# Kernel tuning notes

Hardware: AMD Instinct MI355X
Metric: run time of the kernel (lower is better)

The kernel has to match this reference:

```python
import jax, jax.numpy as jnp
import numpy as np

EPS = 1e-6
BASE_CURVATURE = 1.0


def _artanh(x):
    return jnp.arctanh(jnp.clip(x, -1.0 + 1e-5, 1.0 - 1e-5))


def _norm(x):
    return jnp.maximum(jnp.linalg.norm(x, axis=-1, keepdims=True), EPS)


def _logmap0(x, c):
    # Poincare-ball log map at origin
    sc = jnp.sqrt(c)
    n = _norm(x)
    return _artanh(sc * n) * x / (sc * n)


def _expmap0(v, c):
    # Poincare-ball exp map at origin
    sc = jnp.sqrt(c)
    n = _norm(v)
    return jnp.tanh(sc * n) * v / (sc * n)


def _mobius_add(x, y, c):
    x2 = jnp.sum(x * x, axis=-1, keepdims=True)
    y2 = jnp.sum(y * y, axis=-1, keepdims=True)
    xy = jnp.sum(x * y, axis=-1, keepdims=True)
    num = (1.0 + 2.0 * c * xy + c * y2) * x + (1.0 - c * x2) * y
    den = 1.0 + 2.0 * c * xy + (c * c) * x2 * y2
    return num / jnp.maximum(den, EPS)


def _mobius_scalar_mul(t, x, c):
    sc = jnp.sqrt(c)
    n = _norm(x)
    return jnp.tanh(t * _artanh(sc * n)) * x / (sc * n)


def setup_inputs() -> dict:
    key = jax.random.key(0)
    ks = jax.random.split(key, 8)
    B, D_in, D_out, K = 4096, 2048, 2048, 4
    scale_w = np.sqrt(2.0 / (D_in + D_out)) * 0.1
    return {
        "x": jax.random.normal(ks[0], (B, D_in), jnp.float32) * 0.05,
        "weight": jax.random.normal(ks[1], (D_out, D_in), jnp.float32) * scale_w,
        "bias": jax.random.normal(ks[2], (D_out,), jnp.float32) * 0.01,
        "curv_weight": jax.random.normal(ks[3], (1, D_in), jnp.float32) * 0.1,
        "curv_bias": jnp.zeros((1,), jnp.float32),
        "anchors": jax.random.normal(ks[4], (K, D_out), jnp.float32) * 0.3,
        "t_values": jnp.full((K,), 0.5, jnp.float32),
        "anchor_weights": jnp.full((K,), 1.0 / K, jnp.float32),
    }


def reference(x, weight, bias, curv_weight, curv_bias, anchors, t_values, anchor_weights):
    # 1) dynamic curvature prediction: c_i = base_c * softplus(x . w + b), then mean
    logits = x @ curv_weight[0] + curv_bias[0]                 # [B]
    curvatures = BASE_CURVATURE * jax.nn.softplus(logits)      # [B]
    c = jax.lax.stop_gradient(jnp.mean(curvatures))            # scalar (.item() in torch)

    # 2) fused hyperbolic linear: expmap0(logmap0(x) @ W^T + b)
    u = _logmap0(x, c)                                         # [B, D_in]
    h = u @ weight.T + bias                                    # [B, D_out]
    y = _expmap0(h, c)                                         # [B, D_out]

    # 3) geodesic activation: weighted Mobius geodesic toward each anchor
    xe = y[:, None, :]                                         # [B, 1, D]
    a = anchors[None, :, :]                                    # [1, K, D]
    diff = _mobius_add(-xe, a, c)                              # [B, K, D]
    step = _mobius_scalar_mul(t_values[None, :, None], diff, c)
    g = _mobius_add(xe, step, c)                               # [B, K, D]
    w = jax.nn.softmax(anchor_weights)                         # [K]
    return jnp.einsum("bkd,k->bd", g, w)                       # [B, D_out]
```

## Files before the change

### kernel.cpp

```cpp
#include <hip/hip_runtime.h>
#include <stdint.h>

#define B_ROWS 4096
#define D_IN   2048
#define D_OUT  2048
#define KANCH  4
#define MROWS  8

typedef _Float16 half8  __attribute__((ext_vector_type(8)));
typedef _Float16 half4  __attribute__((ext_vector_type(4)));
typedef float    floatx4 __attribute__((ext_vector_type(4)));
typedef const __attribute__((address_space(1))) uint8_t* gptr_t;
typedef __attribute__((address_space(3))) uint8_t* lptr_t;

__device__ __forceinline__ float frcp(float x)   { return __builtin_amdgcn_rcpf(x); }
__device__ __forceinline__ float ftanh(float x)  { float e = __expf(2.f * x); return (e - 1.f) * frcp(e + 1.f); }
__device__ __forceinline__ float fatanh(float z) { return 0.5f * __logf((1.f + z) * frcp(1.f - z)); }

__global__ __launch_bounds__(256) void k_prep(
    const float* __restrict__ x,
    const float* __restrict__ W,
    const float* __restrict__ cw,
    const float* __restrict__ cb,
    const float* __restrict__ bias,
    const float* __restrict__ anchors,
    _Float16* __restrict__ xh,
    _Float16* __restrict__ Wh,
    float* __restrict__ n2x,
    float* __restrict__ spart,
    float* __restrict__ scal)
{
    int tid = threadIdx.x;
    if (blockIdx.x < 1024) {
        int w = tid >> 6, lane = tid & 63;
        int row = blockIdx.x * 4 + w;
        const floatx4* xr = (const floatx4*)(x + (size_t)row * D_IN);
        const floatx4* wr = (const floatx4*)cw;
        _Float16* xo = xh + (size_t)row * D_IN;
        float dot = 0.f, ss = 0.f;
#pragma unroll
        for (int i = 0; i < 8; ++i) {
            int idx = i * 64 + lane;
            floatx4 xv = xr[idx];
            floatx4 wv = wr[idx];
#pragma unroll
            for (int j = 0; j < 4; ++j) {
                dot += xv[j] * wv[j];
                ss  += xv[j] * xv[j];
            }
            half4 h = {(_Float16)xv[0], (_Float16)xv[1], (_Float16)xv[2], (_Float16)xv[3]};
            *(half4*)(xo + idx * 4) = h;
        }
#pragma unroll
        for (int off = 32; off; off >>= 1) {
            dot += __shfl_down(dot, off);
            ss  += __shfl_down(ss, off);
        }
        __shared__ float spw[4];
        if (lane == 0) {
            n2x[row] = ss;
            float z = dot + cb[0];
            spw[w] = (z > 20.f) ? z : log1pf(expf(z));
        }
        __syncthreads();
        if (tid == 0)
            spart[blockIdx.x] = spw[0] + spw[1] + spw[2] + spw[3];
    } else if (blockIdx.x < 2048) {
        int blk = blockIdx.x - 1024;
        const floatx4* W4 = (const floatx4*)W;
#pragma unroll
        for (int i = 0; i < 4; ++i) {
            int idx = blk * 1024 + i * 256 + tid;
            floatx4 v = W4[idx];
            half4 h = {(_Float16)v[0], (_Float16)v[1], (_Float16)v[2], (_Float16)v[3]};
            *(half4*)(Wh + (size_t)idx * 4) = h;
        }
    } else {
        int w = tid >> 6, lane = tid & 63;
        float bf[8], af[KANCH][8];
        *(floatx4*)(bf)     = *(const floatx4*)(bias + tid * 8);
        *(floatx4*)(bf + 4) = *(const floatx4*)(bias + tid * 8 + 4);
#pragma unroll
        for (int k = 0; k < KANCH; ++k) {
            *(floatx4*)(af[k])     = *(const floatx4*)(anchors + (size_t)k * D_OUT + tid * 8);
            *(floatx4*)(af[k] + 4) = *(const floatx4*)(anchors + (size_t)k * D_OUT + tid * 8 + 4);
        }
        float v[9];
#pragma unroll
        for (int q = 0; q < 9; ++q) v[q] = 0.f;
#pragma unroll
        for (int j = 0; j < 8; ++j) {
            v[0] += bf[j] * bf[j];
#pragma unroll
            for (int k = 0; k < KANCH; ++k) {
                v[1 + k] += bf[j] * af[k][j];
                v[5 + k] += af[k][j] * af[k][j];
            }
        }
#pragma unroll
        for (int off = 32; off; off >>= 1)
#pragma unroll
            for (int q = 0; q < 9; ++q) v[q] += __shfl_down(v[q], off);
        __shared__ float red[4][9];
        if (lane == 0)
#pragma unroll
            for (int q = 0; q < 9; ++q) red[w][q] = v[q];
        __syncthreads();
        if (tid == 0)
#pragma unroll
            for (int q = 0; q < 9; ++q)
                scal[1 + q] = red[0][q] + red[1][q] + red[2][q] + red[3][q];
    }
}

template<int KPB>
__global__ __launch_bounds__(512, 2) void k_gemm(
    const _Float16* __restrict__ A,
    const _Float16* __restrict__ W,
    _Float16* __restrict__ P0,
    _Float16* __restrict__ P1)
{
    constexpr int NT = KPB / 64;
    constexpr int NZ = (KPB == D_IN) ? 1 : 2;
    __shared__ __align__(16) _Float16 lds[2][2][2][8192];
    const int tid  = threadIdx.x;
    const int lane = tid & 63;
    const int w    = tid >> 6;
    const int wm   = w >> 2;
    const int wn   = w & 3;

    int lin = (blockIdx.z * gridDim.y + blockIdx.y) * gridDim.x + blockIdx.x;
    int xcd = lin & 7;
    int i   = lin >> 3;
    int zz, mt, nt;
    if (NZ == 2) {
        zz = xcd & 1;
        int grp = xcd >> 1;
        mt = (grp >> 1) * 8 + (i >> 2);
        nt = (grp & 1) * 4 + (i & 3);
    } else {
        zz = 0;
        mt = (xcd >> 1) * 4 + (i >> 2);
        nt = (xcd & 1) * 4 + (i & 3);
    }
    const int bm0 = mt * 256;
    const int bn0 = nt * 256;
    const int kbase = zz * KPB;
    _Float16* P = (zz == 0) ? P0 : P1;

    const int e0 = tid * 16;
    const int srow = w * 16 + (lane & 15);
    const int scol = (lane >> 4) * 8;
    const size_t asrc = (size_t)(bm0 + srow) * D_IN + scol + kbase;
    const size_t bsrc = (size_t)(bn0 + srow) * D_IN + scol + kbase;
    const int wmoff = wm * 8192;
    const int wnoff = wn * 4096;
    const int loff  = lane * 16;

#define STAGE_Q(OP, D, KH, GP, SRC, KB) do { \
    uint8_t* qb_ = (uint8_t*)&lds[OP][D][KH][0]; \
    __builtin_amdgcn_global_load_lds((gptr_t)((GP) + (SRC) + (KB)), (lptr_t)(qb_ + e0), 16, 0, 0); \
    __builtin_amdgcn_global_load_lds((gptr_t)((GP) + (SRC) + (size_t)128 * D_IN + (KB)), (lptr_t)(qb_ + e0 + 8192), 16, 0, 0); \
} while (0)

    floatx4 acc[8][4];
#pragma unroll
    for (int mi = 0; mi < 8; ++mi)
#pragma unroll
        for (int ni = 0; ni < 4; ++ni)
            acc[mi][ni] = (floatx4){0.f, 0.f, 0.f, 0.f};

    STAGE_Q(0, 0, 0, A, asrc, 0);
    STAGE_Q(0, 0, 1, A, asrc, 32);
    STAGE_Q(1, 0, 0, W, bsrc, 0);
    STAGE_Q(1, 0, 1, W, bsrc, 32);
    STAGE_Q(0, 1, 0, A, asrc, 64);
    STAGE_Q(1, 1, 0, W, bsrc, 64);
    STAGE_Q(1, 1, 1, W, bsrc, 96);
    asm volatile("s_waitcnt vmcnt(6)" ::: "memory");
    __builtin_amdgcn_s_barrier();

    half8 aq[4], bq[4];

#define LOAD_A4(D, KH, MI0) do { _Pragma("unroll") \
    for (int mi = 0; mi < 4; ++mi) \
        aq[mi] = *(const half8*)((const uint8_t*)&lds[0][D][KH][0] + wmoff + ((MI0) + mi) * 1024 + loff); \
} while (0)
#define LOAD_B4(D, KH) do { _Pragma("unroll") \
    for (int ni = 0; ni < 4; ++ni) \
        bq[ni] = *(const half8*)((const uint8_t*)&lds[1][D][KH][0] + wnoff + ni * 1024 + loff); \
} while (0)
#define MFMA16(MI0) do { \
    __builtin_amdgcn_s_barrier(); \
    __builtin_amdgcn_s_setprio(1); \
    _Pragma("unroll") for (int mi = 0; mi < 4; ++mi) \
    _Pragma("unroll") for (int ni = 0; ni < 4; ++ni) \
        acc[(MI0) + mi][ni] = __builtin_amdgcn_mfma_f32_16x16x32_f16(aq[mi], bq[ni], acc[(MI0) + mi][ni], 0, 0, 0); \
    __builtin_amdgcn_s_setprio(0); \
} while (0)
#define ENDPH() __builtin_amdgcn_s_barrier()

#define TILE_BODY(T, D) do { \
    LOAD_A4(D, 0, 0); LOAD_B4(D, 0); \
    if ((T) + 1 < NT) STAGE_Q(0, (D) ^ 1, 1, A, asrc, ((T) + 1) * 64 + 32); \
    MFMA16(0); ENDPH(); \
    LOAD_A4(D, 0, 4); \
    if ((T) + 2 < NT) STAGE_Q(1, D, 0, W, bsrc, ((T) + 2) * 64); \
    MFMA16(4); ENDPH(); \
    LOAD_A4(D, 1, 0); LOAD_B4(D, 1); \
    if ((T) + 2 < NT) STAGE_Q(0, D, 0, A, asrc, ((T) + 2) * 64); \
    MFMA16(0); ENDPH(); \
    LOAD_A4(D, 1, 4); \
    if ((T) + 2 < NT) STAGE_Q(1, D, 1, W, bsrc, ((T) + 2) * 64 + 32); \
    MFMA16(4); \
    if ((T) < NT - 2) asm volatile("s_waitcnt vmcnt(6)" ::: "memory"); \
    else              asm volatile("s_waitcnt vmcnt(0)" ::: "memory"); \
    ENDPH(); \
} while (0)

    for (int t = 0; t < NT; t += 2) {
        TILE_BODY(t, 0);
        TILE_BODY(t + 1, 1);
    }

#undef TILE_BODY
#undef ENDPH
#undef MFMA16
#undef LOAD_B4
#undef LOAD_A4
#undef STAGE_Q

#pragma unroll
    for (int mi = 0; mi < 8; ++mi) {
#pragma unroll
        for (int r = 0; r < 4; ++r) {
            int gm = bm0 + wm * 128 + mi * 16 + (lane >> 4) * 4 + r;
#pragma unroll
            for (int ni = 0; ni < 4; ++ni) {
                int gn = bn0 + wn * 64 + ni * 16 + (lane & 15);
                P[(size_t)gm * D_OUT + gn] = (_Float16)acc[mi][ni][r];
            }
        }
    }
}

__global__ __launch_bounds__(256) void k_mobius(
    const _Float16* __restrict__ P0,
    const _Float16* __restrict__ P1,
    const float* __restrict__ bias,
    const float* __restrict__ anchors,
    const float* __restrict__ tv,
    const float* __restrict__ aw,
    const float* __restrict__ n2x,
    const float* __restrict__ spart,
    const float* __restrict__ scal,
    int split,
    float* __restrict__ out)
{
    int tid = threadIdx.x, w = tid >> 6, lane = tid & 63;
    float bf[8];
    *(floatx4*)(bf)     = *(const floatx4*)(bias + tid * 8);
    *(floatx4*)(bf + 4) = *(const floatx4*)(bias + tid * 8 + 4);
    float af[KANCH][8];
#pragma unroll
    for (int k = 0; k < KANCH; ++k) {
        *(floatx4*)(af[k])     = *(const floatx4*)(anchors + (size_t)k * D_OUT + tid * 8);
        *(floatx4*)(af[k] + 4) = *(const floatx4*)(anchors + (size_t)k * D_OUT + tid * 8 + 4);
    }
    float v6;
    {
        floatx4 s4 = ((const floatx4*)spart)[tid];
        v6 = s4[0] + s4[1] + s4[2] + s4[3];
    }
#pragma unroll
    for (int off = 32; off; off >>= 1) v6 += __shfl_down(v6, off);
    __shared__ float redS[4];
    __shared__ float red[4][6];
    __shared__ float cf[2 + KANCH];
    if (lane == 0) redS[w] = v6;
    __syncthreads();

    int k = lane & 3;
    float c = 0.f, sc = 0.f, wk = 0.f, tvk = 0.f, bb = 0.f, ba = 0.f, aa = 0.f;
    if (w == 0) {
        float spsum = redS[0] + redS[1] + redS[2] + redS[3];
        c  = spsum * (1.0f / (float)B_ROWS);
        sc = __builtin_amdgcn_sqrtf(c);
        float ek = __expf(aw[k]);
        float se = ek;
        se += __shfl_xor(se, 1);
        se += __shfl_xor(se, 2);
        wk = ek * frcp(se);
        tvk = tv[k];
        bb = scal[1];
        ba = scal[2 + k];
        aa = scal[6 + k];
    }

    for (int r = 0; r < MROWS; ++r) {
        int row = blockIdx.x * MROWS + r;
        size_t rowoff = (size_t)row * D_OUT;
        float pf[8];
        {
            half8 p = *(const half8*)(P0 + rowoff + tid * 8);
#pragma unroll
            for (int j = 0; j < 8; ++j) pf[j] = (float)p[j];
        }
        if (split == 2) {
            half8 q = *(const half8*)(P1 + rowoff + tid * 8);
#pragma unroll
            for (int j = 0; j < 8; ++j) pf[j] += (float)q[j];
        }
        float v[6];
#pragma unroll
        for (int q = 0; q < 6; ++q) v[q] = 0.f;
#pragma unroll
        for (int j = 0; j < 8; ++j) {
            v[0] += pf[j] * pf[j];
            v[1] += pf[j] * bf[j];
#pragma unroll
            for (int kk = 0; kk < KANCH; ++kk) v[2 + kk] += pf[j] * af[kk][j];
        }
#pragma unroll
        for (int off = 32; off; off >>= 1)
#pragma unroll
            for (int q = 0; q < 6; ++q) v[q] += __shfl_down(v[q], off);
        if (lane == 0)
#pragma unroll
            for (int q = 0; q < 6; ++q) red[w][q] = v[q];
        __syncthreads();
        if (w == 0) {
            float pp = red[0][0] + red[1][0] + red[2][0] + red[3][0];
            float pb = red[0][1] + red[1][1] + red[2][1] + red[3][1];
            float pa = red[0][2 + k] + red[1][2 + k] + red[2][2 + k] + red[3][2 + k];
            float nx = fmaxf(__builtin_amdgcn_sqrtf(n2x[row]), 1e-6f);
            float ax = sc * nx;
            float zx = fminf(fmaxf(ax, -1.f + 1e-5f), 1.f - 1e-5f);
            float f = fatanh(zx) * frcp(ax);
            float hh = f * f * pp + 2.f * f * pb + bb;
            float ha = f * pa + ba;
            float nh = fmaxf(__builtin_amdgcn_sqrtf(hh), 1e-6f);
            float snh = sc * nh;
            float gy = ftanh(snh) * frcp(snh);
            float x2 = gy * gy * hh;
            float B1 = 1.f - c * x2;
            float y2 = aa;
            float dy = gy * ha;
            float A1 = 1.f - 2.f * c * dy + c * y2;
            float den1 = fmaxf(1.f - 2.f * c * dy + c * c * x2 * y2, 1e-6f);
            float rd1 = frcp(den1);
            float al = -A1 * rd1, be = B1 * rd1;
            float nd2 = fmaxf(al * al * x2 + 2.f * al * be * dy + be * be * y2, 0.f);
            float nd = fmaxf(__builtin_amdgcn_sqrtf(nd2), 1e-6f);
            float snd = sc * nd;
            float zc = fminf(fmaxf(snd, -1.f + 1e-5f), 1.f - 1e-5f);
            float s = ftanh(tvk * fatanh(zc)) * frcp(snd);
            float y2s = s * s * nd2;
            float xys = s * (al * x2 + be * dy);
            float A2 = 1.f + 2.f * c * xys + c * y2s;
            float den2 = fmaxf(1.f + 2.f * c * xys + c * c * x2 * y2s, 1e-6f);
            float rd2 = frcp(den2);
            float Cy  = (A2 + B1 * s * al) * rd2;
            float Cak = (B1 * s * be) * rd2;
            float chk = wk * Cy;
            chk += __shfl_xor(chk, 1);
            chk += __shfl_xor(chk, 2);
            if (lane == 0) {
                float c0 = gy * chk;
                cf[0] = c0 * f;
                cf[1] = c0;
            }
            if (lane < 4) cf[2 + lane] = wk * Cak;
        }
        __syncthreads();
        float cp = cf[0], cb_ = cf[1];
        float o[8];
#pragma unroll
        for (int j = 0; j < 8; ++j) {
            float val = cp * pf[j] + cb_ * bf[j];
#pragma unroll
            for (int kk = 0; kk < KANCH; ++kk) val += cf[2 + kk] * af[kk][j];
            o[j] = val;
        }
        *(floatx4*)(out + rowoff + tid * 8)     = *(floatx4*)(o);
        *(floatx4*)(out + rowoff + tid * 8 + 4) = *(floatx4*)(o + 4);
    }
}

extern "C" void kernel_launch(void* const* d_in, const int* in_sizes, int n_in,
                              void* d_out, int out_size, void* d_ws, size_t ws_size,
                              hipStream_t stream) {
    const float* x       = (const float*)d_in[0];
    const float* wt      = (const float*)d_in[1];
    const float* bias    = (const float*)d_in[2];
    const float* cw      = (const float*)d_in[3];
    const float* cb      = (const float*)d_in[4];
    const float* anchors = (const float*)d_in[5];
    const float* tv      = (const float*)d_in[6];
    const float* aw      = (const float*)d_in[7];
    float* out = (float*)d_out;

    _Float16* Wh = (_Float16*)d_ws;
    _Float16* xh = Wh + (size_t)D_OUT * D_IN;
    float* n2x   = (float*)(xh + (size_t)B_ROWS * D_IN);
    float* spart = n2x + B_ROWS;
    float* scal  = spart + 1024;
    _Float16* P0 = (_Float16*)(scal + 16);
    _Float16* P1 = P0 + (size_t)B_ROWS * D_OUT;
    size_t need2 = (size_t)((char*)(P1 + (size_t)B_ROWS * D_OUT) - (char*)d_ws);
    int split = (ws_size >= need2) ? 2 : 1;

    k_prep<<<2049, 256, 0, stream>>>(x, wt, cw, cb, bias, anchors, xh, Wh, n2x, spart, scal);
    if (split == 2)
        k_gemm<D_IN / 2><<<dim3(8, 16, 2), 512, 0, stream>>>(xh, Wh, P0, P1);
    else
        k_gemm<D_IN><<<dim3(8, 16, 1), 512, 0, stream>>>(xh, Wh, P0, P1);
    k_mobius<<<B_ROWS / MROWS, 256, 0, stream>>>(P0, P1, bias, anchors, tv, aw, n2x, spart, scal, split, out);
}
```

Before: 168.6 us.

## Fuse prep, GEMM and Mobius epilogue into one cooperative kernel with grid syncs

Replaces the three separate launches (prep, split-K GEMM, Mobius epilogue) with a single cooperative kernel of 256 blocks, using grid.sync between phases. Prep work is redistributed so each block converts 16 x-rows and 8 W-rows, and the epilogue processes 16 rows per block with 512 threads. This removes two kernel launch gaps and inter-kernel drain/fill overhead, at the cost of grid-wide barriers and a coarser, less parallel prep and epilogue phase (256 blocks instead of 2049/512). The fallback path keeps separate kernels and adds an extra syncthreads in the Mobius loop.

Result: slower. 266.7 us (+58.2%).

```diff
diff --git a/kernel.cpp b/kernel.cpp
--- a/kernel.cpp
+++ b/kernel.cpp
@@ -1,4 +1,5 @@
 #include <hip/hip_runtime.h>
+#include <hip/hip_cooperative_groups.h>
 #include <stdint.h>
 
 #define B_ROWS 4096
@@ -7,6 +8,8 @@
 #define KANCH  4
 #define MROWS  8
 
+namespace cg = cooperative_groups;
+
 typedef _Float16 half8  __attribute__((ext_vector_type(8)));
 typedef _Float16 half4  __attribute__((ext_vector_type(4)));
 typedef float    floatx4 __attribute__((ext_vector_type(4)));
@@ -17,18 +20,367 @@
 __device__ __forceinline__ float ftanh(float x)  { float e = __expf(2.f * x); return (e - 1.f) * frcp(e + 1.f); }
 __device__ __forceinline__ float fatanh(float z) { return 0.5f * __logf((1.f + z) * frcp(1.f - z)); }
 
-__global__ __launch_bounds__(256) void k_prep(
+__global__ __launch_bounds__(512, 2) void k_mega(
     const float* __restrict__ x,
     const float* __restrict__ W,
+    const float* __restrict__ bias,
     const float* __restrict__ cw,
     const float* __restrict__ cb,
-    const float* __restrict__ bias,
     const float* __restrict__ anchors,
+    const float* __restrict__ tv,
+    const float* __restrict__ aw,
     _Float16* __restrict__ xh,
     _Float16* __restrict__ Wh,
     float* __restrict__ n2x,
     float* __restrict__ spart,
-    float* __restrict__ scal)
+    float* __restrict__ scal,
+    _Float16* __restrict__ P0,
+    _Float16* __restrict__ P1,
+    float* __restrict__ out)
+{
+    __shared__ __align__(16) _Float16 lds[2][2][2][8192];
+    float* scr = (float*)&lds[0][0][0][0];
+
+    const int tid  = threadIdx.x;
+    const int lane = tid & 63;
+    const int w    = tid >> 6;
+    const int lin  = (blockIdx.z * gridDim.y + blockIdx.y) * gridDim.x + blockIdx.x;
+
+    cg::grid_group grid = cg::this_grid();
+
+    {
+        const floatx4* wr4 = (const floatx4*)cw;
+        floatx4 wv[8];
+#pragma unroll
+        for (int i = 0; i < 8; ++i) wv[i] = wr4[i * 64 + lane];
+        float sp = 0.f;
+#pragma unroll
+        for (int rr = 0; rr < 2; ++rr) {
+            int row = lin * 16 + w * 2 + rr;
+            const floatx4* xr = (const floatx4*)(x + (size_t)row * D_IN);
+            _Float16* xo = xh + (size_t)row * D_IN;
+            float dot = 0.f, ss = 0.f;
+#pragma unroll
+            for (int i = 0; i < 8; ++i) {
+                int idx = i * 64 + lane;
+                floatx4 xv = xr[idx];
+#pragma unroll
+                for (int j = 0; j < 4; ++j) {
+                    dot += xv[j] * wv[i][j];
+                    ss  += xv[j] * xv[j];
+                }
+                half4 h = {(_Float16)xv[0], (_Float16)xv[1], (_Float16)xv[2], (_Float16)xv[3]};
+                *(half4*)(xo + idx * 4) = h;
+            }
+#pragma unroll
+            for (int off = 32; off; off >>= 1) {
+                dot += __shfl_down(dot, off);
+                ss  += __shfl_down(ss, off);
+            }
+            if (lane == 0) {
+                n2x[row] = ss;
+                float z = dot + cb[0];
+                sp += (z > 20.f) ? z : log1pf(expf(z));
+            }
+        }
+        if (lane == 0) scr[w] = sp;
+
+        {
+            int wrow = lin * 8 + w;
+            const floatx4* W4 = (const floatx4*)(W + (size_t)wrow * D_IN);
+            _Float16* wo = Wh + (size_t)wrow * D_IN;
+#pragma unroll
+            for (int i = 0; i < 8; ++i) {
+                int idx = i * 64 + lane;
+                floatx4 v = W4[idx];
+                half4 h = {(_Float16)v[0], (_Float16)v[1], (_Float16)v[2], (_Float16)v[3]};
+                *(half4*)(wo + idx * 4) = h;
+            }
+        }
+
+        float v9[9];
+#pragma unroll
+        for (int q = 0; q < 9; ++q) v9[q] = 0.f;
+        if (lin == 0) {
+            floatx4 bv = *(const floatx4*)(bias + tid * 4);
+            floatx4 av[KANCH];
+#pragma unroll
+            for (int k = 0; k < KANCH; ++k)
+                av[k] = *(const floatx4*)(anchors + (size_t)k * D_OUT + tid * 4);
+#pragma unroll
+            for (int j = 0; j < 4; ++j) {
+                v9[0] += bv[j] * bv[j];
+#pragma unroll
+                for (int k = 0; k < KANCH; ++k) {
+                    v9[1 + k] += bv[j] * av[k][j];
+                    v9[5 + k] += av[k][j] * av[k][j];
+                }
+            }
+#pragma unroll
+            for (int off = 32; off; off >>= 1)
+#pragma unroll
+                for (int q = 0; q < 9; ++q) v9[q] += __shfl_down(v9[q], off);
+            if (lane == 0)
+#pragma unroll
+                for (int q = 0; q < 9; ++q) scr[8 + w * 9 + q] = v9[q];
+        }
+        __syncthreads();
+        if (tid == 0) {
+            spart[lin] = scr[0] + scr[1] + scr[2] + scr[3] + scr[4] + scr[5] + scr[6] + scr[7];
+            if (lin == 0) {
+#pragma unroll
+                for (int q = 0; q < 9; ++q) {
+                    float s = 0.f;
+#pragma unroll
+                    for (int ww = 0; ww < 8; ++ww) s += scr[8 + ww * 9 + q];
+                    scal[1 + q] = s;
+                }
+            }
+        }
+    }
+
+    grid.sync();
+
+    {
+        constexpr int KPB = D_IN / 2;
+        constexpr int NT  = KPB / 64;
+        const int wm = w >> 2;
+        const int wn = w & 3;
+
+        int xcd = lin & 7;
+        int i   = lin >> 3;
+        int zz  = xcd & 1;
+        int grp = xcd >> 1;
+        int mt  = (grp >> 1) * 8 + (i >> 2);
+        int nt  = (grp & 1) * 4 + (i & 3);
+        const int bm0 = mt * 256;
+        const int bn0 = nt * 256;
+        const int kbase = zz * KPB;
+        _Float16* P = (zz == 0) ? P0 : P1;
+
+        const int e0 = tid * 16;
+        const int srow = w * 16 + (lane & 15);
+        const int scol = (lane >> 4) * 8;
+        const size_t asrc = (size_t)(bm0 + srow) * D_IN + scol + kbase;
+        const size_t bsrc = (size_t)(bn0 + srow) * D_IN + scol + kbase;
+        const int wmoff = wm * 8192;
+        const int wnoff = wn * 4096;
+        const int loff  = lane * 16;
+
+#define STAGE_Q(OP, D, KH, GP, SRC, KB) do { \
+    uint8_t* qb_ = (uint8_t*)&lds[OP][D][KH][0]; \
+    __builtin_amdgcn_global_load_lds((gptr_t)((GP) + (SRC) + (KB)), (lptr_t)(qb_ + e0), 16, 0, 0); \
+    __builtin_amdgcn_global_load_lds((gptr_t)((GP) + (SRC) + (size_t)128 * D_IN + (KB)), (lptr_t)(qb_ + e0 + 8192), 16, 0, 0); \
+} while (0)
+
+        floatx4 acc[8][4];
+#pragma unroll
+        for (int mi = 0; mi < 8; ++mi)
+#pragma unroll
+            for (int ni = 0; ni < 4; ++ni)
+                acc[mi][ni] = (floatx4){0.f, 0.f, 0.f, 0.f};
+
+        STAGE_Q(0, 0, 0, xh, asrc, 0);
+        STAGE_Q(0, 0, 1, xh, asrc, 32);
+        STAGE_Q(1, 0, 0, Wh, bsrc, 0);
+        STAGE_Q(1, 0, 1, Wh, bsrc, 32);
+        STAGE_Q(0, 1, 0, xh, asrc, 64);
+        STAGE_Q(1, 1, 0, Wh, bsrc, 64);
+        STAGE_Q(1, 1, 1, Wh, bsrc, 96);
+        asm volatile("s_waitcnt vmcnt(6)" ::: "memory");
+        __builtin_amdgcn_s_barrier();
+
+        half8 aq[4], bq[4];
+
+#define LOAD_A4(D, KH, MI0) do { _Pragma("unroll") \
+    for (int mi = 0; mi < 4; ++mi) \
+        aq[mi] = *(const half8*)((const uint8_t*)&lds[0][D][KH][0] + wmoff + ((MI0) + mi) * 1024 + loff); \
+} while (0)
+#define LOAD_B4(D, KH) do { _Pragma("unroll") \
+    for (int ni = 0; ni < 4; ++ni) \
+        bq[ni] = *(const half8*)((const uint8_t*)&lds[1][D][KH][0] + wnoff + ni * 1024 + loff); \
+} while (0)
+#define MFMA16(MI0) do { \
+    __builtin_amdgcn_s_barrier(); \
+    __builtin_amdgcn_s_setprio(1); \
+    _Pragma("unroll") for (int mi = 0; mi < 4; ++mi) \
+    _Pragma("unroll") for (int ni = 0; ni < 4; ++ni) \
+        acc[(MI0) + mi][ni] = __builtin_amdgcn_mfma_f32_16x16x32_f16(aq[mi], bq[ni], acc[(MI0) + mi][ni], 0, 0, 0); \
+    __builtin_amdgcn_s_setprio(0); \
+} while (0)
+#define ENDPH() __builtin_amdgcn_s_barrier()
+
+#define TILE_BODY(T, D) do { \
+    LOAD_A4(D, 0, 0); LOAD_B4(D, 0); \
+    if ((T) + 1 < NT) STAGE_Q(0, (D) ^ 1, 1, xh, asrc, ((T) + 1) * 64 + 32); \
+    MFMA16(0); ENDPH(); \
+    LOAD_A4(D, 0, 4); \
+    if ((T) + 2 < NT) STAGE_Q(1, D, 0, Wh, bsrc, ((T) + 2) * 64); \
+    MFMA16(4); ENDPH(); \
+    LOAD_A4(D, 1, 0); LOAD_B4(D, 1); \
+    if ((T) + 2 < NT) STAGE_Q(0, D, 0, xh, asrc, ((T) + 2) * 64); \
+    MFMA16(0); ENDPH(); \
+    LOAD_A4(D, 1, 4); \
+    if ((T) + 2 < NT) STAGE_Q(1, D, 1, Wh, bsrc, ((T) + 2) * 64 + 32); \
+    MFMA16(4); \
+    if ((T) < NT - 2) asm volatile("s_waitcnt vmcnt(6)" ::: "memory"); \
+    else              asm volatile("s_waitcnt vmcnt(0)" ::: "memory"); \
+    ENDPH(); \
+} while (0)
+
+        for (int t = 0; t < NT; t += 2) {
+            TILE_BODY(t, 0);
+            TILE_BODY(t + 1, 1);
+        }
+
+#undef TILE_BODY
+#undef ENDPH
+#undef MFMA16
+#undef LOAD_B4
+#undef LOAD_A4
+#undef STAGE_Q
+
+#pragma unroll
+        for (int mi = 0; mi < 8; ++mi) {
+#pragma unroll
+            for (int r = 0; r < 4; ++r) {
+                int gm = bm0 + wm * 128 + mi * 16 + (lane >> 4) * 4 + r;
+#pragma unroll
+                for (int ni = 0; ni < 4; ++ni) {
+                    int gn = bn0 + wn * 64 + ni * 16 + (lane & 15);
+                    P[(size_t)gm * D_OUT + gn] = (_Float16)acc[mi][ni][r];
+                }
+            }
+        }
+    }
+
+    grid.sync();
+
+    {
+        float bf4[4];
+        *(floatx4*)bf4 = *(const floatx4*)(bias + tid * 4);
+        float af4[KANCH][4];
+#pragma unroll
+        for (int k = 0; k < KANCH; ++k)
+            *(floatx4*)af4[k] = *(const floatx4*)(anchors + (size_t)k * D_OUT + tid * 4);
+
+        int k = lane & 3;
+        float c = 0.f, sc = 0.f, wk = 0.f, tvk = 0.f, bb = 0.f, ba = 0.f, aa = 0.f;
+        if (w == 0) {
+            floatx4 s4 = ((const floatx4*)spart)[lane];
+            float v6 = s4[0] + s4[1] + s4[2] + s4[3];
+#pragma unroll
+            for (int off = 32; off; off >>= 1) v6 += __shfl_down(v6, off);
+            float spsum = __shfl(v6, 0);
+            c  = spsum * (1.0f / (float)B_ROWS);
+            sc = __builtin_amdgcn_sqrtf(c);
+            float ek = __expf(aw[k]);
+            float se = ek;
+            se += __shfl_xor(se, 1);
+            se += __shfl_xor(se, 2);
+            wk = ek * frcp(se);
+            tvk = tv[k];
+            bb = scal[1];
+            ba = scal[2 + k];
+            aa = scal[6 + k];
+        }
+
+        for (int r = 0; r < 16; ++r) {
+            int row = lin * 16 + r;
+            size_t rowoff = (size_t)row * D_OUT;
+            float pf[4];
+            {
+                half4 p0 = *(const half4*)(P0 + rowoff + tid * 4);
+                half4 p1 = *(const half4*)(P1 + rowoff + tid * 4);
+#pragma unroll
+                for (int j = 0; j < 4; ++j) pf[j] = (float)p0[j] + (float)p1[j];
+            }
+            float v[6];
+#pragma unroll
+            for (int q = 0; q < 6; ++q) v[q] = 0.f;
+#pragma unroll
+            for (int j = 0; j < 4; ++j) {
+                v[0] += pf[j] * pf[j];
+                v[1] += pf[j] * bf4[j];
+#pragma unroll
+                for (int kk = 0; kk < KANCH; ++kk) v[2 + kk] += pf[j] * af4[kk][j];
+            }
+#pragma unroll
+            for (int off = 32; off; off >>= 1)
+#pragma unroll
+                for (int q = 0; q < 6; ++q) v[q] += __shfl_down(v[q], off);
+            if (lane == 0)
+#pragma unroll
+                for (int q = 0; q < 6; ++q) scr[8 + w * 6 + q] = v[q];
+            __syncthreads();
+            if (w == 0) {
+                float pp = 0.f, pb = 0.f, pa = 0.f;
+#pragma unroll
+                for (int ww = 0; ww < 8; ++ww) {
+                    pp += scr[8 + ww * 6 + 0];
+                    pb += scr[8 + ww * 6 + 1];
+                    pa += scr[8 + ww * 6 + 2 + k];
+                }
+                float nx = fmaxf(__builtin_amdgcn_sqrtf(n2x[row]), 1e-6f);
+                float ax = sc * nx;
+                float zx = fminf(fmaxf(ax, -1.f + 1e-5f), 1.f - 1e-5f);
+                float f = fatanh(zx) * frcp(ax);
+                float hh = f * f * pp + 2.f * f * pb + bb;
+                float ha = f * pa + ba;
+                float nh = fmaxf(__builtin_amdgcn_sqrtf(hh), 1e-6f);
+                float snh = sc * nh;
+                float gy = ftanh(snh) * frcp(snh);
+                float x2 = gy * gy * hh;
+                float B1 = 1.f - c * x2;
+                float y2 = aa;
+                float dy = gy * ha;
+                float A1 = 1.f - 2.f * c * dy + c * y2;
+                float den1 = fmaxf(1.f - 2.f * c * dy + c * c * x2 * y2, 1e-6f);
+                float rd1 = frcp(den1);
+                float al = -A1 * rd1, be = B1 * rd1;
+                float nd2 = fmaxf(al * al * x2 + 2.f * al * be * dy + be * be * y2, 0.f);
+                float nd = fmaxf(__builtin_amdgcn_sqrtf(nd2), 1e-6f);
+                float snd = sc * nd;
+                float zc = fminf(fmaxf(snd, -1.f + 1e-5f), 1.f - 1e-5f);
+                float s = ftanh(tvk * fatanh(zc)) * frcp(snd);
+                float y2s = s * s * nd2;
+                float xys = s * (al * x2 + be * dy);
+                float A2 = 1.f + 2.f * c * xys + c * y2s;
+                float den2 = fmaxf(1.f + 2.f * c * xys + c * c * x2 * y2s, 1e-6f);
+                float rd2 = frcp(den2);
+                float Cy  = (A2 + B1 * s * al) * rd2;
+                float Cak = (B1 * s * be) * rd2;
+                float chk = wk * Cy;
+                chk += __shfl_xor(chk, 1);
+                chk += __shfl_xor(chk, 2);
+                if (lane == 0) {
+                    float c0 = gy * chk;
+                    scr[0] = c0 * f;
+                    scr[1] = c0;
+                }
+                if (lane < 4) scr[2 + lane] = wk * Cak;
+            }
+            __syncthreads();
+            float cp = scr[0], cb_ = scr[1];
+            float o[4];
+#pragma unroll
+            for (int j = 0; j < 4; ++j) {
+                float val = cp * pf[j] + cb_ * bf4[j];
+#pragma unroll
+                for (int kk = 0; kk < KANCH; ++kk) val += scr[2 + kk] * af4[kk][j];
+                o[j] = val;
+            }
+            *(floatx4*)(out + rowoff + tid * 4) = *(floatx4*)o;
+        }
+    }
+}
+
+__global__ __launch_bounds__(256) void k_prep(
+    const float* __restrict__ x, const float* __restrict__ W,
+    const float* __restrict__ cw, const float* __restrict__ cb,
+    const float* __restrict__ bias, const float* __restrict__ anchors,
+    _Float16* __restrict__ xh, _Float16* __restrict__ Wh,
+    float* __restrict__ n2x, float* __restrict__ spart, float* __restrict__ scal)
 {
     int tid = threadIdx.x;
     if (blockIdx.x < 1024) {
@@ -44,18 +396,12 @@
             floatx4 xv = xr[idx];
             floatx4 wv = wr[idx];
 #pragma unroll
-            for (int j = 0; j < 4; ++j) {
-                dot += xv[j] * wv[j];
-                ss  += xv[j] * xv[j];
-            }
+            for (int j = 0; j < 4; ++j) { dot += xv[j] * wv[j]; ss += xv[j] * xv[j]; }
             half4 h = {(_Float16)xv[0], (_Float16)xv[1], (_Float16)xv[2], (_Float16)xv[3]};
             *(half4*)(xo + idx * 4) = h;
         }
 #pragma unroll
-        for (int off = 32; off; off >>= 1) {
-            dot += __shfl_down(dot, off);
-            ss  += __shfl_down(ss, off);
-        }
+        for (int off = 32; off; off >>= 1) { dot += __shfl_down(dot, off); ss += __shfl_down(ss, off); }
         __shared__ float spw[4];
         if (lane == 0) {
             n2x[row] = ss;
@@ -63,8 +409,7 @@
             spw[w] = (z > 20.f) ? z : log1pf(expf(z));
         }
         __syncthreads();
-        if (tid == 0)
-            spart[blockIdx.x] = spw[0] + spw[1] + spw[2] + spw[3];
+        if (tid == 0) spart[blockIdx.x] = spw[0] + spw[1] + spw[2] + spw[3];
     } else if (blockIdx.x < 2048) {
         int blk = blockIdx.x - 1024;
         const floatx4* W4 = (const floatx4*)W;
@@ -113,149 +458,12 @@
     }
 }
 
-template<int KPB>
-__global__ __launch_bounds__(512, 2) void k_gemm(
-    const _Float16* __restrict__ A,
-    const _Float16* __restrict__ W,
-    _Float16* __restrict__ P0,
-    _Float16* __restrict__ P1)
-{
-    constexpr int NT = KPB / 64;
-    constexpr int NZ = (KPB == D_IN) ? 1 : 2;
-    __shared__ __align__(16) _Float16 lds[2][2][2][8192];
-    const int tid  = threadIdx.x;
-    const int lane = tid & 63;
-    const int w    = tid >> 6;
-    const int wm   = w >> 2;
-    const int wn   = w & 3;
-
-    int lin = (blockIdx.z * gridDim.y + blockIdx.y) * gridDim.x + blockIdx.x;
-    int xcd = lin & 7;
-    int i   = lin >> 3;
-    int zz, mt, nt;
-    if (NZ == 2) {
-        zz = xcd & 1;
-        int grp = xcd >> 1;
-        mt = (grp >> 1) * 8 + (i >> 2);
-        nt = (grp & 1) * 4 + (i & 3);
-    } else {
-        zz = 0;
-        mt = (xcd >> 1) * 4 + (i >> 2);
-        nt = (xcd & 1) * 4 + (i & 3);
-    }
-    const int bm0 = mt * 256;
-    const int bn0 = nt * 256;
-    const int kbase = zz * KPB;
-    _Float16* P = (zz == 0) ? P0 : P1;
-
-    const int e0 = tid * 16;
-    const int srow = w * 16 + (lane & 15);
-    const int scol = (lane >> 4) * 8;
-    const size_t asrc = (size_t)(bm0 + srow) * D_IN + scol + kbase;
-    const size_t bsrc = (size_t)(bn0 + srow) * D_IN + scol + kbase;
-    const int wmoff = wm * 8192;
-    const int wnoff = wn * 4096;
-    const int loff  = lane * 16;
-
-#define STAGE_Q(OP, D, KH, GP, SRC, KB) do { \
-    uint8_t* qb_ = (uint8_t*)&lds[OP][D][KH][0]; \
-    __builtin_amdgcn_global_load_lds((gptr_t)((GP) + (SRC) + (KB)), (lptr_t)(qb_ + e0), 16, 0, 0); \
-    __builtin_amdgcn_global_load_lds((gptr_t)((GP) + (SRC) + (size_t)128 * D_IN + (KB)), (lptr_t)(qb_ + e0 + 8192), 16, 0, 0); \
-} while (0)
-
-    floatx4 acc[8][4];
-#pragma unroll
-    for (int mi = 0; mi < 8; ++mi)
-#pragma unroll
-        for (int ni = 0; ni < 4; ++ni)
-            acc[mi][ni] = (floatx4){0.f, 0.f, 0.f, 0.f};
-
-    STAGE_Q(0, 0, 0, A, asrc, 0);
-    STAGE_Q(0, 0, 1, A, asrc, 32);
-    STAGE_Q(1, 0, 0, W, bsrc, 0);
-    STAGE_Q(1, 0, 1, W, bsrc, 32);
-    STAGE_Q(0, 1, 0, A, asrc, 64);
-    STAGE_Q(1, 1, 0, W, bsrc, 64);
-    STAGE_Q(1, 1, 1, W, bsrc, 96);
-    asm volatile("s_waitcnt vmcnt(6)" ::: "memory");
-    __builtin_amdgcn_s_barrier();
-
-    half8 aq[4], bq[4];
-
-#define LOAD_A4(D, KH, MI0) do { _Pragma("unroll") \
-    for (int mi = 0; mi < 4; ++mi) \
-        aq[mi] = *(const half8*)((const uint8_t*)&lds[0][D][KH][0] + wmoff + ((MI0) + mi) * 1024 + loff); \
-} while (0)
-#define LOAD_B4(D, KH) do { _Pragma("unroll") \
-    for (int ni = 0; ni < 4; ++ni) \
-        bq[ni] = *(const half8*)((const uint8_t*)&lds[1][D][KH][0] + wnoff + ni * 1024 + loff); \
-} while (0)
-#define MFMA16(MI0) do { \
-    __builtin_amdgcn_s_barrier(); \
-    __builtin_amdgcn_s_setprio(1); \
-    _Pragma("unroll") for (int mi = 0; mi < 4; ++mi) \
-    _Pragma("unroll") for (int ni = 0; ni < 4; ++ni) \
-        acc[(MI0) + mi][ni] = __builtin_amdgcn_mfma_f32_16x16x32_f16(aq[mi], bq[ni], acc[(MI0) + mi][ni], 0, 0, 0); \
-    __builtin_amdgcn_s_setprio(0); \
-} while (0)
-#define ENDPH() __builtin_amdgcn_s_barrier()
-
-#define TILE_BODY(T, D) do { \
-    LOAD_A4(D, 0, 0); LOAD_B4(D, 0); \
-    if ((T) + 1 < NT) STAGE_Q(0, (D) ^ 1, 1, A, asrc, ((T) + 1) * 64 + 32); \
-    MFMA16(0); ENDPH(); \
-    LOAD_A4(D, 0, 4); \
-    if ((T) + 2 < NT) STAGE_Q(1, D, 0, W, bsrc, ((T) + 2) * 64); \
-    MFMA16(4); ENDPH(); \
-    LOAD_A4(D, 1, 0); LOAD_B4(D, 1); \
-    if ((T) + 2 < NT) STAGE_Q(0, D, 0, A, asrc, ((T) + 2) * 64); \
-    MFMA16(0); ENDPH(); \
-    LOAD_A4(D, 1, 4); \
-    if ((T) + 2 < NT) STAGE_Q(1, D, 1, W, bsrc, ((T) + 2) * 64 + 32); \
-    MFMA16(4); \
-    if ((T) < NT - 2) asm volatile("s_waitcnt vmcnt(6)" ::: "memory"); \
-    else              asm volatile("s_waitcnt vmcnt(0)" ::: "memory"); \
-    ENDPH(); \
-} while (0)
-
-    for (int t = 0; t < NT; t += 2) {
-        TILE_BODY(t, 0);
-        TILE_BODY(t + 1, 1);
-    }
-
-#undef TILE_BODY
-#undef ENDPH
-#undef MFMA16
-#undef LOAD_B4
-#undef LOAD_A4
-#undef STAGE_Q
-
-#pragma unroll
-    for (int mi = 0; mi < 8; ++mi) {
-#pragma unroll
-        for (int r = 0; r < 4; ++r) {
-            int gm = bm0 + wm * 128 + mi * 16 + (lane >> 4) * 4 + r;
-#pragma unroll
-            for (int ni = 0; ni < 4; ++ni) {
-                int gn = bn0 + wn * 64 + ni * 16 + (lane & 15);
-                P[(size_t)gm * D_OUT + gn] = (_Float16)acc[mi][ni][r];
-            }
-        }
-    }
-}
-
 __global__ __launch_bounds__(256) void k_mobius(
-    const _Float16* __restrict__ P0,
-    const _Float16* __restrict__ P1,
-    const float* __restrict__ bias,
-    const float* __restrict__ anchors,
-    const float* __restrict__ tv,
-    const float* __restrict__ aw,
-    const float* __restrict__ n2x,
-    const float* __restrict__ spart,
-    const float* __restrict__ scal,
-    int split,
-    float* __restrict__ out)
+    const _Float16* __restrict__ P0, const _Float16* __restrict__ P1,
+    const float* __restrict__ bias, const float* __restrict__ anchors,
+    const float* __restrict__ tv, const float* __restrict__ aw,
+    const float* __restrict__ n2x, const float* __restrict__ spart,
+    const float* __restrict__ scal, int split, float* __restrict__ out)
 {
     int tid = threadIdx.x, w = tid >> 6, lane = tid & 63;
     float bf[8];
@@ -279,7 +487,6 @@
     __shared__ float cf[2 + KANCH];
     if (lane == 0) redS[w] = v6;
     __syncthreads();
-
     int k = lane & 3;
     float c = 0.f, sc = 0.f, wk = 0.f, tvk = 0.f, bb = 0.f, ba = 0.f, aa = 0.f;
     if (w == 0) {
@@ -292,11 +499,8 @@
         se += __shfl_xor(se, 2);
         wk = ek * frcp(se);
         tvk = tv[k];
-        bb = scal[1];
-        ba = scal[2 + k];
-        aa = scal[6 + k];
-    }
-
+        bb = scal[1]; ba = scal[2 + k]; aa = scal[6 + k];
+    }
     for (int r = 0; r < MROWS; ++r) {
         int row = blockIdx.x * MROWS + r;
         size_t rowoff = (size_t)row * D_OUT;
@@ -384,6 +588,126 @@
         }
         *(floatx4*)(out + rowoff + tid * 8)     = *(floatx4*)(o);
         *(floatx4*)(out + rowoff + tid * 8 + 4) = *(floatx4*)(o + 4);
+        __syncthreads();
+    }
+}
+
+template<int KPB>
+__global__ __launch_bounds__(512, 2) void k_gemm(
+    const _Float16* __restrict__ A, const _Float16* __restrict__ W,
+    _Float16* __restrict__ P0, _Float16* __restrict__ P1)
+{
+    constexpr int NT = KPB / 64;
+    __shared__ __align__(16) _Float16 lds[2][2][2][8192];
+    const int tid  = threadIdx.x;
+    const int lane = tid & 63;
+    const int w    = tid >> 6;
+    const int wm   = w >> 2;
+    const int wn   = w & 3;
+    int lin = (blockIdx.z * gridDim.y + blockIdx.y) * gridDim.x + blockIdx.x;
+    int xcd = lin & 7;
+    int i   = lin >> 3;
+    int zz = 0, mt, nt;
+    mt = (xcd >> 1) * 4 + (i >> 2);
+    nt = (xcd & 1) * 4 + (i & 3);
+    const int bm0 = mt * 256;
+    const int bn0 = nt * 256;
+    const int kbase = zz * KPB;
+    _Float16* P = P0;
+
+    const int e0 = tid * 16;
+    const int srow = w * 16 + (lane & 15);
+    const int scol = (lane >> 4) * 8;
+    const size_t asrc = (size_t)(bm0 + srow) * D_IN + scol + kbase;
+    const size_t bsrc = (size_t)(bn0 + srow) * D_IN + scol + kbase;
+    const int wmoff = wm * 8192;
+    const int wnoff = wn * 4096;
+    const int loff  = lane * 16;
+
+#define STAGE_Q(OP, D, KH, GP, SRC, KB) do { \
+    uint8_t* qb_ = (uint8_t*)&lds[OP][D][KH][0]; \
+    __builtin_amdgcn_global_load_lds((gptr_t)((GP) + (SRC) + (KB)), (lptr_t)(qb_ + e0), 16, 0, 0); \
+    __builtin_amdgcn_global_load_lds((gptr_t)((GP) + (SRC) + (size_t)128 * D_IN + (KB)), (lptr_t)(qb_ + e0 + 8192), 16, 0, 0); \
+} while (0)
+
+    floatx4 acc[8][4];
+#pragma unroll
+    for (int mi = 0; mi < 8; ++mi)
+#pragma unroll
+        for (int ni = 0; ni < 4; ++ni)
+            acc[mi][ni] = (floatx4){0.f, 0.f, 0.f, 0.f};
+
+    STAGE_Q(0, 0, 0, A, asrc, 0);
+    STAGE_Q(0, 0, 1, A, asrc, 32);
+    STAGE_Q(1, 0, 0, W, bsrc, 0);
+    STAGE_Q(1, 0, 1, W, bsrc, 32);
+    STAGE_Q(0, 1, 0, A, asrc, 64);
+    STAGE_Q(1, 1, 0, W, bsrc, 64);
+    STAGE_Q(1, 1, 1, W, bsrc, 96);
+    asm volatile("s_waitcnt vmcnt(6)" ::: "memory");
+    __builtin_amdgcn_s_barrier();
+
+    half8 aq[4], bq[4];
+
+#define LOAD_A4(D, KH, MI0) do { _Pragma("unroll") \
+    for (int mi = 0; mi < 4; ++mi) \
+        aq[mi] = *(const half8*)((const uint8_t*)&lds[0][D][KH][0] + wmoff + ((MI0) + mi) * 1024 + loff); \
+} while (0)
+#define LOAD_B4(D, KH) do { _Pragma("unroll") \
+    for (int ni = 0; ni < 4; ++ni) \
+        bq[ni] = *(const half8*)((const uint8_t*)&lds[1][D][KH][0] + wnoff + ni * 1024 + loff); \
+} while (0)
+#define MFMA16(MI0) do { \
+    __builtin_amdgcn_s_barrier(); \
+    __builtin_amdgcn_s_setprio(1); \
+    _Pragma("unroll") for (int mi = 0; mi < 4; ++mi) \
+    _Pragma("unroll") for (int ni = 0; ni < 4; ++ni) \
+        acc[(MI0) + mi][ni] = __builtin_amdgcn_mfma_f32_16x16x32_f16(aq[mi], bq[ni], acc[(MI0) + mi][ni], 0, 0, 0); \
+    __builtin_amdgcn_s_setprio(0); \
+} while (0)
+#define ENDPH() __builtin_amdgcn_s_barrier()
+
+#define TILE_BODY(T, D) do { \
+    LOAD_A4(D, 0, 0); LOAD_B4(D, 0); \
+    if ((T) + 1 < NT) STAGE_Q(0, (D) ^ 1, 1, A, asrc, ((T) + 1) * 64 + 32); \
+    MFMA16(0); ENDPH(); \
+    LOAD_A4(D, 0, 4); \
+    if ((T) + 2 < NT) STAGE_Q(1, D, 0, W, bsrc, ((T) + 2) * 64); \
+    MFMA16(4); ENDPH(); \
+    LOAD_A4(D, 1, 0); LOAD_B4(D, 1); \
+    if ((T) + 2 < NT) STAGE_Q(0, D, 0, A, asrc, ((T) + 2) * 64); \
+    MFMA16(0); ENDPH(); \
+    LOAD_A4(D, 1, 4); \
+    if ((T) + 2 < NT) STAGE_Q(1, D, 1, W, bsrc, ((T) + 2) * 64 + 32); \
+    MFMA16(4); \
+    if ((T) < NT - 2) asm volatile("s_waitcnt vmcnt(6)" ::: "memory"); \
+    else              asm volatile("s_waitcnt vmcnt(0)" ::: "memory"); \
+    ENDPH(); \
+} while (0)
+
+    for (int t = 0; t < NT; t += 2) {
+        TILE_BODY(t, 0);
+        TILE_BODY(t + 1, 1);
+    }
+
+#undef TILE_BODY
+#undef ENDPH
+#undef MFMA16
+#undef LOAD_B4
+#undef LOAD_A4
+#undef STAGE_Q
+
+#pragma unroll
+    for (int mi = 0; mi < 8; ++mi) {
+#pragma unroll
+        for (int r = 0; r < 4; ++r) {
+            int gm = bm0 + wm * 128 + mi * 16 + (lane >> 4) * 4 + r;
+#pragma unroll
+            for (int ni = 0; ni < 4; ++ni) {
+                int gn = bn0 + wn * 64 + ni * 16 + (lane & 15);
+                P[(size_t)gm * D_OUT + gn] = (_Float16)acc[mi][ni][r];
+            }
+        }
     }
 }
 
@@ -408,12 +732,18 @@
     _Float16* P0 = (_Float16*)(scal + 16);
     _Float16* P1 = P0 + (size_t)B_ROWS * D_OUT;
     size_t need2 = (size_t)((char*)(P1 + (size_t)B_ROWS * D_OUT) - (char*)d_ws);
-    int split = (ws_size >= need2) ? 2 : 1;
-
-    k_prep<<<2049, 256, 0, stream>>>(x, wt, cw, cb, bias, anchors, xh, Wh, n2x, spart, scal);
-    if (split == 2)
-        k_gemm<D_IN / 2><<<dim3(8, 16, 2), 512, 0, stream>>>(xh, Wh, P0, P1);
-    else
+
+    if (ws_size >= need2) {
+        void* args[] = {
+            (void*)&x, (void*)&wt, (void*)&bias, (void*)&cw, (void*)&cb,
+            (void*)&anchors, (void*)&tv, (void*)&aw,
+            (void*)&xh, (void*)&Wh, (void*)&n2x, (void*)&spart, (void*)&scal,
+            (void*)&P0, (void*)&P1, (void*)&out };
+        hipLaunchCooperativeKernel((const void*)k_mega, dim3(8, 16, 2), dim3(512),
+                                   args, 0, stream);
+    } else {
+        k_prep<<<2049, 256, 0, stream>>>(x, wt, cw, cb, bias, anchors, xh, Wh, n2x, spart, scal);
         k_gemm<D_IN><<<dim3(8, 16, 1), 512, 0, stream>>>(xh, Wh, P0, P1);
-    k_mobius<<<B_ROWS / MROWS, 256, 0, stream>>>(P0, P1, bias, anchors, tv, aw, n2x, spart, scal, split, out);
+        k_mobius<<<B_ROWS / MROWS, 256, 0, stream>>>(P0, P1, bias, anchors, tv, aw, n2x, spart, scal, 1, out);
+    }
 }
```
